# Kernel tuning notes

Hardware: AMD Instinct MI355X
Metric: run time of the kernel (lower is better)

Reference implementation:

```python
import jax, jax.numpy as jnp
import numpy as np
import math

B, S, D = 4, 2048, 1024

def setup_inputs() -> dict:
    key = jax.random.key(0)
    k1, k2, k3, k4 = jax.random.split(key, 4)
    scale = 1.0 / math.sqrt(D)
    return {
        "x": jax.random.normal(k1, (B, S, D), dtype=jnp.float32),
        "w_q": jax.random.normal(k2, (D, D), dtype=jnp.float32) * scale,
        "w_k": jax.random.normal(k3, (D, D), dtype=jnp.float32) * scale,
        "w_v": jax.random.normal(k4, (D, D), dtype=jnp.float32) * scale,
        "causal": 1,
    }

def reference(x, w_q, w_k, w_v, causal):
    # QKV projections: nn.Linear(dim, dim, bias=False) -> x @ W.T
    q = jnp.einsum('bsd,ed->bse', x, w_q)
    k = jnp.einsum('bsd,ed->bse', x, w_k)
    v = jnp.einsum('bsd,ed->bse', x, w_v)
    d_k = q.shape[-1]
    scores = jnp.einsum('bqd,bkd->bqk', q, k) / jnp.sqrt(jnp.asarray(d_k, q.dtype))
    if causal:
        seq_len = q.shape[-2]
        mask = jnp.triu(jnp.ones((seq_len, seq_len), dtype=bool), k=1)
        scores = jnp.where(mask, jnp.asarray(-jnp.inf, scores.dtype), scores)
    weights = jax.nn.softmax(scores, axis=-1)
    return jnp.einsum('bqk,bkd->bqd', weights, v)
```

## Files before the change

### kernel.cpp

```cpp
#include <hip/hip_runtime.h>
#include <stdint.h>

typedef unsigned short u16;
typedef __attribute__((ext_vector_type(8))) __bf16 bf16x8;
typedef __attribute__((ext_vector_type(4))) float f32x4;

__device__ __forceinline__ u16 f2bf(float f) {
  unsigned u = __float_as_uint(f);
  u += 0x7FFF + ((u >> 16) & 1);
  return (u16)(u >> 16);
}

__device__ __forceinline__ float bf2f(u16 h) {
  return __uint_as_float(((unsigned)h) << 16);
}

__device__ __forceinline__ void llds16(const u16* g, u16* l) {
  __builtin_amdgcn_global_load_lds(
      (const __attribute__((address_space(1))) void*)g,
      (__attribute__((address_space(3))) void*)l, 16, 0, 0);
}

__global__ __launch_bounds__(256) void cast_all(
    const float* __restrict__ x, const float* __restrict__ wq,
    const float* __restrict__ wk, const float* __restrict__ wv,
    u16* __restrict__ xb, u16* __restrict__ wb) {
  int i = blockIdx.x * 256 + threadIdx.x;
  const float* src; u16* dst; int off;
  if (i < 2097152)      { src = x;  dst = xb;            off = i; }
  else if (i < 2359296) { src = wq; dst = wb;            off = i - 2097152; }
  else if (i < 2621440) { src = wk; dst = wb + 1048576;  off = i - 2359296; }
  else                  { src = wv; dst = wb + 2097152;  off = i - 2621440; }
  float4 f = ((const float4*)src)[off];
  ushort4 o;
  o.x = f2bf(f.x); o.y = f2bf(f.y); o.z = f2bf(f.z); o.w = f2bf(f.w);
  ((ushort4*)dst)[off] = o;
}

template<int MODE>
__global__ __launch_bounds__(256) void gemm_nt(
    const u16* __restrict__ A, long long sA, int lda,
    const u16* __restrict__ B, long long sB, int ldb,
    void* __restrict__ Cp, long long sC, int ldc,
    int K, u16* __restrict__ vt, float scale,
    const float* __restrict__ linv, const int* __restrict__ causalp) {
  const int t = threadIdx.x;
  const int causal = (MODE == 0) ? 1 : causalp[0];

  int rt = blockIdx.x, ct = blockIdx.y;
  if (MODE == 1) {
    int x = blockIdx.x;
    if (x < 136) {
      int r = (int)((sqrtf(8.0f * x + 1.0f) - 1.0f) * 0.5f);
      while ((r + 1) * (r + 2) / 2 <= x) ++r;
      while (r * (r + 1) / 2 > x) --r;
      rt = r; ct = x - r * (r + 1) / 2;
    } else {
      int y = x - 136;
      int r = (int)((sqrtf(8.0f * y + 1.0f) - 1.0f) * 0.5f);
      while ((r + 1) * (r + 2) / 2 <= y) ++r;
      while (r * (r + 1) / 2 > y) --r;
      int c = y - r * (r + 1) / 2;
      rt = c; ct = r + 1;
      if (causal) return;
    }
  }
  if (MODE == 2) rt = 15 - blockIdx.x;

  const int rowbase = rt * 128;
  const int colbase = ct * 128;
  const u16* Ab = A + (long long)blockIdx.z * sA;
  const u16* Bb = B + (long long)blockIdx.z * sB;

  int Keff = K;
  if (MODE == 2 && causal) Keff = min(K, rowbase + 128);

  __shared__ u16 As[8192];
  __shared__ u16 Bs[8192];

  const int lane = t & 63;
  const int wv = t >> 6;
  const int wr = wv >> 1;
  const int wc = wv & 1;
  const int quad = lane >> 4;
  const int lr = lane & 15;

  f32x4 acc[4][4];
  const f32x4 zero = {0.f, 0.f, 0.f, 0.f};
#pragma unroll
  for (int i = 0; i < 4; ++i)
#pragma unroll
    for (int j = 0; j < 4; ++j) acc[i][j] = zero;

  {
    const int csw = (t & 7) ^ ((t >> 3) & 7);
    const u16* ga = Ab + (long long)(rowbase + (t >> 3)) * lda + csw * 8;
    const u16* gb = Bb + (long long)(colbase + (t >> 3)) * ldb + csw * 8;
    const long long ra = 32LL * lda, rb = 32LL * ldb;
    u16* la = As + t * 8;
    u16* lb = Bs + t * 8;

    const int m7 = lr & 7;
    const int a_base = (wr * 64 + lr) * 64 + ((quad ^ m7) * 8);
    const int b_base = (wc * 64 + lr) * 64 + ((quad ^ m7) * 8);

    for (int k0 = 0; k0 < Keff; k0 += 64) {
      __syncthreads();
#pragma unroll
      for (int i = 0; i < 4; ++i) {
        llds16(ga + k0 + i * ra, la + i * 2048);
        llds16(gb + k0 + i * rb, lb + i * 2048);
      }
      __syncthreads();
#pragma unroll
      for (int ks = 0; ks < 2; ++ks) {
        const int ko = ks ? 32 : 0;
        bf16x8 af[4], bfv[4];
#pragma unroll
        for (int tm = 0; tm < 4; ++tm)
          af[tm] = *(const bf16x8*)(As + ((a_base + tm * 1024) ^ ko));
#pragma unroll
        for (int tn = 0; tn < 4; ++tn)
          bfv[tn] = *(const bf16x8*)(Bs + ((b_base + tn * 1024) ^ ko));
#pragma unroll
        for (int tm = 0; tm < 4; ++tm)
#pragma unroll
          for (int tn = 0; tn < 4; ++tn)
            acc[tm][tn] = __builtin_amdgcn_mfma_f32_16x16x32_bf16(
                af[tm], bfv[tn], acc[tm][tn], 0, 0, 0);
      }
    }
  }

  if (MODE == 0 && colbase >= 2048) {
#pragma unroll
    for (int tm = 0; tm < 4; ++tm) {
      int s0 = rowbase + wr * 64 + tm * 16 + quad * 4;
      int b = s0 >> 11;
      int sl = s0 & 2047;
#pragma unroll
      for (int tn = 0; tn < 4; ++tn) {
        int e = colbase - 2048 + wc * 64 + tn * 16 + lr;
        ushort4 o;
        o.x = f2bf(acc[tm][tn][0]);
        o.y = f2bf(acc[tm][tn][1]);
        o.z = f2bf(acc[tm][tn][2]);
        o.w = f2bf(acc[tm][tn][3]);
        *(ushort4*)(vt + ((long long)(b * 1024 + e)) * 2048 + sl) = o;
      }
    }
    return;
  }

#pragma unroll
  for (int tm = 0; tm < 4; ++tm) {
#pragma unroll
    for (int r = 0; r < 4; ++r) {
      int grow = rowbase + wr * 64 + tm * 16 + quad * 4 + r;
      float li;
      if (MODE == 2) li = linv[blockIdx.z * 2048 + grow];
#pragma unroll
      for (int tn = 0; tn < 4; ++tn) {
        int gcol = colbase + wc * 64 + tn * 16 + lr;
        float val = acc[tm][tn][r];
        if (MODE == 0) {
          ((u16*)Cp)[(long long)grow * ldc + gcol] = f2bf(val);
        } else if (MODE == 1) {
          u16* C = (u16*)Cp + (long long)blockIdx.z * sC;
          float ex = (causal && gcol > grow) ? 0.f : __expf(val * scale);
          C[(long long)grow * ldc + gcol] = f2bf(ex);
        } else {
          float* C = (float*)Cp + (long long)blockIdx.z * sC;
          C[(long long)grow * ldc + gcol] = val * li;
        }
      }
    }
  }
}

__global__ __launch_bounds__(256) void rowsum(
    const u16* __restrict__ S, float* __restrict__ linv,
    const int* __restrict__ causalp) {
  const long long row = blockIdx.x;
  const int rloc = blockIdx.x & 2047;
  const int colmax = causalp[0] ? ((rloc | 127) + 1) : 2048;
  const u16* rp = S + row * 2048;
  const int t = threadIdx.x;
  const int lane = t & 63;
  const int wv = t >> 6;
  __shared__ float red[4];

  float sm = 0.f;
  if (t * 8 < colmax) {
    union { uint4 u; u16 s[8]; } raw;
    raw.u = *(const uint4*)(rp + t * 8);
#pragma unroll
    for (int i = 0; i < 8; ++i) sm += bf2f(raw.s[i]);
  }
  for (int o = 32; o > 0; o >>= 1) sm += __shfl_xor(sm, o, 64);
  if (lane == 0) red[wv] = sm;
  __syncthreads();
  if (t == 0) linv[row] = 1.0f / (red[0] + red[1] + red[2] + red[3]);
}

extern "C" void kernel_launch(void* const* d_in, const int* in_sizes, int n_in,
                              void* d_out, int out_size, void* d_ws, size_t ws_size,
                              hipStream_t stream) {
  const float* x  = (const float*)d_in[0];
  const float* wq = (const float*)d_in[1];
  const float* wk = (const float*)d_in[2];
  const float* wv = (const float*)d_in[3];
  const int* causal = (const int*)d_in[4];
  float* out = (float*)d_out;

  char* ws = (char*)d_ws;
  u16* xb = (u16*)(ws);
  u16* wb = (u16*)(ws + 16777216);
  u16* qk = (u16*)(ws + 23068672);
  u16* vt = (u16*)(ws + 56623104);
  u16* sb = (u16*)(ws + 73400320);
  float* linv = (float*)ws;

  cast_all<<<11264, 256, 0, stream>>>(x, wq, wk, wv, xb, wb);

  gemm_nt<0><<<dim3(64, 24, 1), 256, 0, stream>>>(
      xb, 0, 1024, wb, 0, 1024, qk, 0, 2048, 1024, vt, 1.0f, nullptr, causal);

  gemm_nt<1><<<dim3(256, 1, 4), 256, 0, stream>>>(
      qk, 2048LL * 2048, 2048, qk + 1024, 2048LL * 2048, 2048,
      sb, 2048LL * 2048, 2048, 1024, nullptr, 0.03125f, nullptr, causal);

  rowsum<<<8192, 256, 0, stream>>>(sb, linv, causal);

  gemm_nt<2><<<dim3(16, 8, 4), 256, 0, stream>>>(
      sb, 2048LL * 2048, 2048, vt, 1024LL * 2048, 2048,
      out, 2048LL * 1024, 1024, 2048, nullptr, 1.0f, linv, causal);
}
```

Before: 240.6 us.

## Switch GEMMs to 32x32 MFMA and fuse softmax row sums via atomics

Replaces the 16x16x32 MFMA tiling with 32x32x16 bf16 MFMA, using 2x2 accumulators of 16 floats per wave and remapped LDS fragment addressing and epilogue indexing. The separate rowsum kernel is removed. The exp-score GEMM now reduces each row's partial sums across lanes and atomically adds them into a zeroed lsum buffer, and the final GEMM applies a hardware reciprocal. This removes one launch and a full re-read of the score matrix, at the cost of atomic contention, nondeterministic summation order and an approximate reciprocal.

```diff
diff --git a/kernel.cpp b/kernel.cpp
--- a/kernel.cpp
+++ b/kernel.cpp
@@ -3,7 +3,7 @@
 
 typedef unsigned short u16;
 typedef __attribute__((ext_vector_type(8))) __bf16 bf16x8;
-typedef __attribute__((ext_vector_type(4))) float f32x4;
+typedef __attribute__((ext_vector_type(16))) float f32x16;
 
 __device__ __forceinline__ u16 f2bf(float f) {
   unsigned u = __float_as_uint(f);
@@ -24,8 +24,9 @@
 __global__ __launch_bounds__(256) void cast_all(
     const float* __restrict__ x, const float* __restrict__ wq,
     const float* __restrict__ wk, const float* __restrict__ wv,
-    u16* __restrict__ xb, u16* __restrict__ wb) {
+    u16* __restrict__ xb, u16* __restrict__ wb, float* __restrict__ lsum) {
   int i = blockIdx.x * 256 + threadIdx.x;
+  if (i < 8192) lsum[i] = 0.f;
   const float* src; u16* dst; int off;
   if (i < 2097152)      { src = x;  dst = xb;            off = i; }
   else if (i < 2359296) { src = wq; dst = wb;            off = i - 2097152; }
@@ -43,7 +44,7 @@
     const u16* __restrict__ B, long long sB, int ldb,
     void* __restrict__ Cp, long long sC, int ldc,
     int K, u16* __restrict__ vt, float scale,
-    const float* __restrict__ linv, const int* __restrict__ causalp) {
+    float* __restrict__ lsum, const int* __restrict__ causalp) {
   const int t = threadIdx.x;
   const int causal = (MODE == 0) ? 1 : causalp[0];
 
@@ -79,18 +80,20 @@
   __shared__ u16 Bs[8192];
 
   const int lane = t & 63;
-  const int wv = t >> 6;
-  const int wr = wv >> 1;
-  const int wc = wv & 1;
-  const int quad = lane >> 4;
-  const int lr = lane & 15;
-
-  f32x4 acc[4][4];
-  const f32x4 zero = {0.f, 0.f, 0.f, 0.f};
-#pragma unroll
-  for (int i = 0; i < 4; ++i)
-#pragma unroll
-    for (int j = 0; j < 4; ++j) acc[i][j] = zero;
+  const int wid = t >> 6;
+  const int wr = wid >> 1;
+  const int wc = wid & 1;
+  const int l31 = lane & 31;
+  const int lh  = lane >> 5;
+  const int m7  = lane & 7;
+
+  f32x16 acc[2][2];
+#pragma unroll
+  for (int i = 0; i < 2; ++i)
+#pragma unroll
+    for (int j = 0; j < 2; ++j)
+#pragma unroll
+      for (int e = 0; e < 16; ++e) acc[i][j][e] = 0.f;
 
   {
     const int csw = (t & 7) ^ ((t >> 3) & 7);
@@ -100,9 +103,8 @@
     u16* la = As + t * 8;
     u16* lb = Bs + t * 8;
 
-    const int m7 = lr & 7;
-    const int a_base = (wr * 64 + lr) * 64 + ((quad ^ m7) * 8);
-    const int b_base = (wc * 64 + lr) * 64 + ((quad ^ m7) * 8);
+    const int a_base = (wr * 64 + l31) * 64 + ((lh ^ m7) * 8);
+    const int b_base = (wc * 64 + l31) * 64 + ((lh ^ m7) * 8);
 
     for (int k0 = 0; k0 < Keff; k0 += 64) {
       __syncthreads();
@@ -113,20 +115,20 @@
       }
       __syncthreads();
 #pragma unroll
-      for (int ks = 0; ks < 2; ++ks) {
-        const int ko = ks ? 32 : 0;
-        bf16x8 af[4], bfv[4];
-#pragma unroll
-        for (int tm = 0; tm < 4; ++tm)
-          af[tm] = *(const bf16x8*)(As + ((a_base + tm * 1024) ^ ko));
-#pragma unroll
-        for (int tn = 0; tn < 4; ++tn)
-          bfv[tn] = *(const bf16x8*)(Bs + ((b_base + tn * 1024) ^ ko));
-#pragma unroll
-        for (int tm = 0; tm < 4; ++tm)
-#pragma unroll
-          for (int tn = 0; tn < 4; ++tn)
-            acc[tm][tn] = __builtin_amdgcn_mfma_f32_16x16x32_bf16(
+      for (int ks = 0; ks < 4; ++ks) {
+        const int ko = ks * 16;
+        bf16x8 af[2], bfv[2];
+#pragma unroll
+        for (int tm = 0; tm < 2; ++tm)
+          af[tm] = *(const bf16x8*)(As + ((a_base + tm * 2048) ^ ko));
+#pragma unroll
+        for (int tn = 0; tn < 2; ++tn)
+          bfv[tn] = *(const bf16x8*)(Bs + ((b_base + tn * 2048) ^ ko));
+#pragma unroll
+        for (int tm = 0; tm < 2; ++tm)
+#pragma unroll
+          for (int tn = 0; tn < 2; ++tn)
+            acc[tm][tn] = __builtin_amdgcn_mfma_f32_32x32x16_bf16(
                 af[tm], bfv[tn], acc[tm][tn], 0, 0, 0);
       }
     }
@@ -134,73 +136,62 @@
 
   if (MODE == 0 && colbase >= 2048) {
 #pragma unroll
-    for (int tm = 0; tm < 4; ++tm) {
-      int s0 = rowbase + wr * 64 + tm * 16 + quad * 4;
-      int b = s0 >> 11;
-      int sl = s0 & 2047;
-#pragma unroll
-      for (int tn = 0; tn < 4; ++tn) {
-        int e = colbase - 2048 + wc * 64 + tn * 16 + lr;
-        ushort4 o;
-        o.x = f2bf(acc[tm][tn][0]);
-        o.y = f2bf(acc[tm][tn][1]);
-        o.z = f2bf(acc[tm][tn][2]);
-        o.w = f2bf(acc[tm][tn][3]);
-        *(ushort4*)(vt + ((long long)(b * 1024 + e)) * 2048 + sl) = o;
+    for (int tm = 0; tm < 2; ++tm) {
+#pragma unroll
+      for (int g = 0; g < 4; ++g) {
+        int s0 = rowbase + wr * 64 + tm * 32 + g * 8 + lh * 4;
+        int b = s0 >> 11;
+        int sl = s0 & 2047;
+#pragma unroll
+        for (int tn = 0; tn < 2; ++tn) {
+          int e = colbase - 2048 + wc * 64 + tn * 32 + l31;
+          ushort4 o;
+          o.x = f2bf(acc[tm][tn][g * 4 + 0]);
+          o.y = f2bf(acc[tm][tn][g * 4 + 1]);
+          o.z = f2bf(acc[tm][tn][g * 4 + 2]);
+          o.w = f2bf(acc[tm][tn][g * 4 + 3]);
+          *(ushort4*)(vt + ((long long)(b * 1024 + e)) * 2048 + sl) = o;
+        }
       }
     }
     return;
   }
 
 #pragma unroll
-  for (int tm = 0; tm < 4; ++tm) {
-#pragma unroll
-    for (int r = 0; r < 4; ++r) {
-      int grow = rowbase + wr * 64 + tm * 16 + quad * 4 + r;
-      float li;
-      if (MODE == 2) li = linv[blockIdx.z * 2048 + grow];
-#pragma unroll
-      for (int tn = 0; tn < 4; ++tn) {
-        int gcol = colbase + wc * 64 + tn * 16 + lr;
-        float val = acc[tm][tn][r];
-        if (MODE == 0) {
-          ((u16*)Cp)[(long long)grow * ldc + gcol] = f2bf(val);
-        } else if (MODE == 1) {
-          u16* C = (u16*)Cp + (long long)blockIdx.z * sC;
-          float ex = (causal && gcol > grow) ? 0.f : __expf(val * scale);
-          C[(long long)grow * ldc + gcol] = f2bf(ex);
-        } else {
-          float* C = (float*)Cp + (long long)blockIdx.z * sC;
-          C[(long long)grow * ldc + gcol] = val * li;
+  for (int tm = 0; tm < 2; ++tm) {
+#pragma unroll
+    for (int g = 0; g < 4; ++g) {
+#pragma unroll
+      for (int rr = 0; rr < 4; ++rr) {
+        const int r = g * 4 + rr;
+        const int grow = rowbase + wr * 64 + tm * 32 + rr + g * 8 + lh * 4;
+        float li, rsum = 0.f;
+        if (MODE == 2) li = __builtin_amdgcn_rcpf(lsum[blockIdx.z * 2048 + grow]);
+#pragma unroll
+        for (int tn = 0; tn < 2; ++tn) {
+          const int gcol = colbase + wc * 64 + tn * 32 + l31;
+          float val = acc[tm][tn][r];
+          if (MODE == 0) {
+            ((u16*)Cp)[(long long)grow * ldc + gcol] = f2bf(val);
+          } else if (MODE == 1) {
+            u16* C = (u16*)Cp + (long long)blockIdx.z * sC;
+            float ex = (causal && gcol > grow) ? 0.f : __expf(val * scale);
+            C[(long long)grow * ldc + gcol] = f2bf(ex);
+            rsum += ex;
+          } else {
+            float* C = (float*)Cp + (long long)blockIdx.z * sC;
+            C[(long long)grow * ldc + gcol] = val * li;
+          }
         }
-      }
-    }
-  }
-}
-
-__global__ __launch_bounds__(256) void rowsum(
-    const u16* __restrict__ S, float* __restrict__ linv,
-    const int* __restrict__ causalp) {
-  const long long row = blockIdx.x;
-  const int rloc = blockIdx.x & 2047;
-  const int colmax = causalp[0] ? ((rloc | 127) + 1) : 2048;
-  const u16* rp = S + row * 2048;
-  const int t = threadIdx.x;
-  const int lane = t & 63;
-  const int wv = t >> 6;
-  __shared__ float red[4];
-
-  float sm = 0.f;
-  if (t * 8 < colmax) {
-    union { uint4 u; u16 s[8]; } raw;
-    raw.u = *(const uint4*)(rp + t * 8);
-#pragma unroll
-    for (int i = 0; i < 8; ++i) sm += bf2f(raw.s[i]);
-  }
-  for (int o = 32; o > 0; o >>= 1) sm += __shfl_xor(sm, o, 64);
-  if (lane == 0) red[wv] = sm;
-  __syncthreads();
-  if (t == 0) linv[row] = 1.0f / (red[0] + red[1] + red[2] + red[3]);
+        if (MODE == 1) {
+#pragma unroll
+          for (int o = 16; o > 0; o >>= 1) rsum += __shfl_xor(rsum, o, 64);
+          if (l31 == 0)
+            atomicAdd(&lsum[blockIdx.z * 2048 + grow], rsum);
+        }
+      }
+    }
+  }
 }
 
 extern "C" void kernel_launch(void* const* d_in, const int* in_sizes, int n_in,
@@ -219,20 +210,18 @@
   u16* qk = (u16*)(ws + 23068672);
   u16* vt = (u16*)(ws + 56623104);
   u16* sb = (u16*)(ws + 73400320);
-  float* linv = (float*)ws;
-
-  cast_all<<<11264, 256, 0, stream>>>(x, wq, wk, wv, xb, wb);
+  float* lsum = (float*)(ws + 106954752);
+
+  cast_all<<<11264, 256, 0, stream>>>(x, wq, wk, wv, xb, wb, lsum);
 
   gemm_nt<0><<<dim3(64, 24, 1), 256, 0, stream>>>(
       xb, 0, 1024, wb, 0, 1024, qk, 0, 2048, 1024, vt, 1.0f, nullptr, causal);
 
   gemm_nt<1><<<dim3(256, 1, 4), 256, 0, stream>>>(
       qk, 2048LL * 2048, 2048, qk + 1024, 2048LL * 2048, 2048,
-      sb, 2048LL * 2048, 2048, 1024, nullptr, 0.03125f, nullptr, causal);
-
-  rowsum<<<8192, 256, 0, stream>>>(sb, linv, causal);
+      sb, 2048LL * 2048, 2048, 1024, nullptr, 0.03125f, lsum, causal);
 
   gemm_nt<2><<<dim3(16, 8, 4), 256, 0, stream>>>(
       sb, 2048LL * 2048, 2048, vt, 1024LL * 2048, 2048,
-      out, 2048LL * 1024, 1024, 2048, nullptr, 1.0f, linv, causal);
-}
+      out, 2048LL * 1024, 1024, 2048, nullptr, 1.0f, lsum, causal);
+}
```

New measurement: 241.8 us. Within noise of the previous version (+0.5%).
